# Performance work log

Measured on AMD Instinct MI355X. Metric: run time of the kernel, lower is better.

The kernel has to match this reference:

```python
import jax, jax.numpy as jnp
import numpy as np
import math

KEY_DIM = 16
COMPAT_FACTOR = 1.0 / math.sqrt(KEY_DIM)


def setup_inputs() -> dict:
    key = jax.random.key(0)
    k1, k2, k3, k4, k5 = jax.random.split(key, 5)
    B, G, D, H, K, V = 4, 2048, 128, 8, 16, 16
    h = jax.random.normal(k1, (B, G, D), dtype=jnp.float32)
    # mask: 1 = masked-out (attention forced to zero), 0 = attend
    mask = jax.random.randint(k2, (G, G), 0, 2, dtype=jnp.int32)
    # xavier_uniform over (input_dim, key_dim) fan per head
    lim_qk = math.sqrt(6.0 / (D + K))
    lim_v = math.sqrt(6.0 / (D + V))
    W_Q = jax.random.uniform(k3, (H, D, K), jnp.float32, -lim_qk, lim_qk)
    W_K = jax.random.uniform(k4, (H, D, K), jnp.float32, -lim_qk, lim_qk)
    W_V = jax.random.uniform(k5, (H, D, V), jnp.float32, -lim_v, lim_v)
    return {"h": h, "mask": mask, "W_Q": W_Q, "W_K": W_K, "W_V": W_V}


def reference(h, mask, W_Q, W_K, W_V):
    # h: [B, G, D]; W_Q/W_K: [H, D, K]; W_V: [H, D, V]; mask: [G, G] (1 = masked)
    q = jnp.einsum("bgd,hdk->bhgk", h, W_Q)  # [B, H, G, K]
    k = jnp.einsum("bgd,hdk->bhgk", h, W_K)  # [B, H, G, K]
    v = jnp.einsum("bgd,hdv->bhgv", h, W_V)  # [B, H, G, V]
    compat = COMPAT_FACTOR * jnp.einsum("bhqk,bhgk->bhqg", q, k)  # [B, H, G, G]
    masked = (mask > 0)[None, None, :, :]  # broadcast over batch, heads
    neg = jnp.finfo(compat.dtype).min
    compat = jnp.where(masked, neg, compat)
    attn = jax.nn.softmax(compat, axis=-1)
    # post-softmax hard zeroing at masked positions (as in the original)
    attn = jnp.where(masked, jnp.zeros((), attn.dtype), attn)
    h_p = jnp.einsum("bhqg,bhgv->bhqv", attn, v)  # [B, H, G, V]
    return h_p
```

## Files before the change

kernel.cpp:

```cpp
#include <hip/hip_runtime.h>
#include <hip/hip_bf16.h>

#define GG 2048
#define DD 128
#define HH 8
#define BH 32

typedef _Float16 h2 __attribute__((ext_vector_type(2)));
typedef _Float16 h4 __attribute__((ext_vector_type(4)));
typedef _Float16 h8 __attribute__((ext_vector_type(8)));
typedef __attribute__((ext_vector_type(4))) float f32x4;
typedef unsigned short u16;
typedef unsigned int   u32;
typedef unsigned char  u8;
typedef unsigned long long u64;

#define QSCALE 0.36067376022224085f

#define OFF_Q 0u
#define OFF_K (2u << 20)
#define OFF_V (4u << 20)
#define OFF_M (6u << 20)
#define OFF_H 6815744u
#define OFF_W 8912896u

#if __has_builtin(__builtin_amdgcn_exp2f)
#define EXP2F(x) __builtin_amdgcn_exp2f(x)
#else
#define EXP2F(x) exp2f(x)
#endif

#define MFMA16(a, b, c) __builtin_amdgcn_mfma_f32_16x16x16f16(a, b, c, 0, 0, 0)

__global__ __launch_bounds__(256) void prep_kernel(
    const float* __restrict__ h, const int* __restrict__ mask,
    const float* __restrict__ WQ, const float* __restrict__ WK,
    const float* __restrict__ WV,
    _Float16* __restrict__ hF, _Float16* __restrict__ Wc, u8* __restrict__ mbt)
{
  const int blk = blockIdx.x, tid = threadIdx.x;
  if (blk < 512) {
    int i = (blk * 256 + tid) * 8;
    float4 a = *(const float4*)(h + i);
    float4 b = *(const float4*)(h + i + 4);
    h8 o = { (_Float16)a.x, (_Float16)a.y, (_Float16)a.z, (_Float16)a.w,
             (_Float16)b.x, (_Float16)b.y, (_Float16)b.z, (_Float16)b.w };
    *(h8*)(hF + i) = o;
  } else if (blk < 704) {
    int j = (blk - 512) * 256 + tid;
    int hh = j / (48 * DD);
    int r  = j % (48 * DD);
    int n  = r / DD;
    int d  = r % DD;
    float val;
    if (n < 16)      val = WQ[((size_t)hh * DD + d) * 16 + n] * QSCALE;
    else if (n < 32) val = WK[((size_t)hh * DD + d) * 16 + (n - 16)];
    else             val = WV[((size_t)hh * DD + d) * 16 + (n - 32)];
    Wc[j] = (_Float16)val;
  } else {
    int t = (blk - 704) * 256 + tid;
    const int* m = mask + (size_t)t * 8;
    int4 m0 = *(const int4*)m;
    int4 m1 = *(const int4*)(m + 4);
    u32 byte = (m0.x > 0) | ((m0.y > 0) << 1) | ((m0.z > 0) << 2) | ((m0.w > 0) << 3)
             | ((m1.x > 0) << 4) | ((m1.y > 0) << 5) | ((m1.z > 0) << 6) | ((m1.w > 0) << 7);
    int q  = t >> 8;
    int k8 = t & 255;
    mbt[(size_t)(k8 >> 4) * (GG * 16) + (size_t)q * 16 + (k8 & 15)] = (u8)byte;
  }
}

__global__ __launch_bounds__(64) void proj_mfma(
    const _Float16* __restrict__ hF, const _Float16* __restrict__ Wc,
    _Float16* __restrict__ Qh, _Float16* __restrict__ Kh, _Float16* __restrict__ Vt)
{
  const int bh = blockIdx.x >> 5;
  const int gt = blockIdx.x & 31;
  const int b  = bh >> 3;
  const int hh = bh & (HH - 1);
  const int lane = threadIdx.x;
  const int col  = lane & 15;
  const int quad = lane >> 4;
  const int g0 = gt * 64;

  const _Float16* hb = hF + (size_t)b * GG * DD;
  const _Float16* W  = Wc + (size_t)hh * 48 * DD;

  f32x4 acc[4][3];
  #pragma unroll
  for (int mt = 0; mt < 4; ++mt)
    #pragma unroll
    for (int nt = 0; nt < 3; ++nt)
      acc[mt][nt] = (f32x4){0.f, 0.f, 0.f, 0.f};

  #pragma unroll
  for (int s = 0; s < 4; ++s) {
    h8 a[4], bw[3];
    #pragma unroll
    for (int mt = 0; mt < 4; ++mt)
      a[mt] = *(const h8*)(hb + (size_t)(g0 + mt * 16 + col) * DD + s * 32 + quad * 8);
    #pragma unroll
    for (int nt = 0; nt < 3; ++nt)
      bw[nt] = *(const h8*)(W + (size_t)(nt * 16 + col) * DD + s * 32 + quad * 8);
    #pragma unroll
    for (int mt = 0; mt < 4; ++mt)
      #pragma unroll
      for (int nt = 0; nt < 3; ++nt)
        acc[mt][nt] = __builtin_amdgcn_mfma_f32_16x16x32_f16(a[mt], bw[nt], acc[mt][nt], 0, 0, 0);
  }

  #pragma unroll
  for (int mt = 0; mt < 4; ++mt) {
    #pragma unroll
    for (int r = 0; r < 4; ++r) {
      int g = g0 + mt * 16 + quad * 4 + r;
      Qh[((size_t)bh * GG + g) * 16 + col] = (_Float16)acc[mt][0][r];
      Kh[((size_t)bh * GG + g) * 16 + col] = (_Float16)acc[mt][1][r];
      Vt[((size_t)bh * 16 + col) * GG + g] = (_Float16)acc[mt][2][r];
    }
  }
}

__global__ __launch_bounds__(256) void attn_kernel(
    const _Float16* __restrict__ Qh, const _Float16* __restrict__ Kh,
    const _Float16* __restrict__ Vt, const u8* __restrict__ mbt,
    float* __restrict__ out)
{
  const int tid = threadIdx.x, wave = tid >> 6, lane = tid & 63;
  const int col = lane & 15, quad = lane >> 4;
  const int bh = blockIdx.x & 31;
  const int qb = (blockIdx.x >> 5) * 128 + wave * 32;

  const h4 qf0 = *(const h4*)(Qh + ((size_t)bh * GG + qb + col) * 16 + quad * 4);
  const h4 qf1 = *(const h4*)(Qh + ((size_t)bh * GG + qb + 16 + col) * 16 + quad * 4);

  const _Float16* Kb = Kh + (size_t)bh * GG * 16;
  const _Float16* Vb = Vt + ((size_t)bh * 16 + col) * GG;
  const u8* mr0 = mbt + (size_t)(qb + col) * 16;
  const u8* mr1 = mbt + (size_t)(qb + 16 + col) * 16;

  f32x4 acc0 = {0.f,0.f,0.f,0.f}, acc1 = {0.f,0.f,0.f,0.f};
  const f32x4 cinit = {-4.f, -4.f, -4.f, -4.f};
  float ls0 = 0.f, ls1 = 0.f;
  const int shq = quad * 4;

  for (int g8 = 0; g8 < 16; ++g8) {
    const size_t goff = (size_t)g8 * (GG * 16);
    uint4 mv0 = *(const uint4*)(mr0 + goff);
    uint4 mv1 = *(const uint4*)(mr1 + goff);
    u64 wa0 = (u64)mv0.x | ((u64)mv0.y << 32);
    u64 wa1 = (u64)mv0.z | ((u64)mv0.w << 32);
    u64 wb0 = (u64)mv1.x | ((u64)mv1.y << 32);
    u64 wb1 = (u64)mv1.z | ((u64)mv1.w << 32);

    h4 kf[8], vf[8];
    #pragma unroll
    for (int t = 0; t < 8; ++t) {
      const int kb = g8 * 128 + t * 16;
      kf[t] = *(const h4*)(Kb + (size_t)(kb + col) * 16 + shq);
      vf[t] = *(const h4*)(Vb + kb + shq);
    }

    #pragma unroll
    for (int t = 0; t < 8; ++t) {
      f32x4 s0 = MFMA16(kf[t], qf0, cinit);
      f32x4 s1 = MFMA16(kf[t], qf1, cinit);
      const int sh = (t & 3) * 16 + shq;
      u32 b0 = (u32)(((t < 4) ? wa0 : wa1) >> sh) & 0xFu;
      u32 b1 = (u32)(((t < 4) ? wb0 : wb1) >> sh) & 0xFu;

      float a0 = (b0 & 1u) ? 0.f : EXP2F(s0[0]);
      float a1 = (b0 & 2u) ? 0.f : EXP2F(s0[1]);
      float a2 = (b0 & 4u) ? 0.f : EXP2F(s0[2]);
      float a3 = (b0 & 8u) ? 0.f : EXP2F(s0[3]);
      float c0 = (b1 & 1u) ? 0.f : EXP2F(s1[0]);
      float c1 = (b1 & 2u) ? 0.f : EXP2F(s1[1]);
      float c2 = (b1 & 4u) ? 0.f : EXP2F(s1[2]);
      float c3 = (b1 & 8u) ? 0.f : EXP2F(s1[3]);
      ls0 += (a0 + a1) + (a2 + a3);
      ls1 += (c0 + c1) + (c2 + c3);

      h2 pa01 = __builtin_bit_cast(h2, __builtin_amdgcn_cvt_pkrtz(a0, a1));
      h2 pa23 = __builtin_bit_cast(h2, __builtin_amdgcn_cvt_pkrtz(a2, a3));
      h4 pf0 = __builtin_shufflevector(pa01, pa23, 0, 1, 2, 3);
      h2 pc01 = __builtin_bit_cast(h2, __builtin_amdgcn_cvt_pkrtz(c0, c1));
      h2 pc23 = __builtin_bit_cast(h2, __builtin_amdgcn_cvt_pkrtz(c2, c3));
      h4 pf1 = __builtin_shufflevector(pc01, pc23, 0, 1, 2, 3);

      acc0 = MFMA16(vf[t], pf0, acc0);
      acc1 = MFMA16(vf[t], pf1, acc1);
    }
  }

  float l0 = ls0; l0 += __shfl_xor(l0, 16, 64); l0 += __shfl_xor(l0, 32, 64);
  float l1 = ls1; l1 += __shfl_xor(l1, 16, 64); l1 += __shfl_xor(l1, 32, 64);
  float r0 = (l0 > 0.f) ? (1.f / l0) : 0.f;
  float r1 = (l1 > 0.f) ? (1.f / l1) : 0.f;

  float4 o0 = { acc0[0] * r0, acc0[1] * r0, acc0[2] * r0, acc0[3] * r0 };
  float4 o1 = { acc1[0] * r1, acc1[1] * r1, acc1[2] * r1, acc1[3] * r1 };
  *(float4*)(out + ((size_t)bh * GG + qb + col) * 16 + quad * 4) = o0;
  *(float4*)(out + ((size_t)bh * GG + qb + 16 + col) * 16 + quad * 4) = o1;
}

extern "C" void kernel_launch(void* const* d_in, const int* in_sizes, int n_in,
                              void* d_out, int out_size, void* d_ws, size_t ws_size,
                              hipStream_t stream) {
  const float* h    = (const float*)d_in[0];
  const int*   mask = (const int*)d_in[1];
  const float* WQ   = (const float*)d_in[2];
  const float* WK   = (const float*)d_in[3];
  const float* WV   = (const float*)d_in[4];
  float* out = (float*)d_out;
  char* ws = (char*)d_ws;
  _Float16* Qh = (_Float16*)(ws + OFF_Q);
  _Float16* Kh = (_Float16*)(ws + OFF_K);
  _Float16* Vt = (_Float16*)(ws + OFF_V);
  u8*       mbt = (u8*)(ws + OFF_M);
  _Float16* hF = (_Float16*)(ws + OFF_H);
  _Float16* Wc = (_Float16*)(ws + OFF_W);

  hipLaunchKernelGGL(prep_kernel, dim3(2752), dim3(256), 0, stream,
                     h, mask, WQ, WK, WV, hF, Wc, mbt);
  hipLaunchKernelGGL(proj_mfma, dim3(BH * (GG / 64)), dim3(64), 0, stream,
                     hF, Wc, Qh, Kh, Vt);
  hipLaunchKernelGGL(attn_kernel, dim3(BH * (GG / 128)), dim3(256), 0, stream,
                     Qh, Kh, Vt, mbt, out);
}
```

Baseline: 123.6 us.

## Split attention key range across two wave groups and sum row totals via MFMA

The attention block grows to 512 threads: each group of four waves processes half of the key range for the same query rows, and the partial outputs and row sums are combined through shared memory after a barrier. The row-sum accumulation moves from scalar adds plus cross-lane shuffles to an extra MFMA against a ones vector. This doubles the number of waves available to hide latency on a grid of only 512 blocks. In exchange it doubles the MFMA count in the inner loop and adds an LDS reduction and a barrier.

Result: slower. 126.4 us (+2.3%).

```diff
diff --git a/kernel.cpp b/kernel.cpp
--- a/kernel.cpp
+++ b/kernel.cpp
@@ -121,15 +121,19 @@
   }
 }
 
-__global__ __launch_bounds__(256) void attn_kernel(
+__global__ __launch_bounds__(512, 4) void attn_kernel(
     const _Float16* __restrict__ Qh, const _Float16* __restrict__ Kh,
     const _Float16* __restrict__ Vt, const u8* __restrict__ mbt,
     float* __restrict__ out)
 {
-  const int tid = threadIdx.x, wave = tid >> 6, lane = tid & 63;
+  __shared__ float Lacc[4][32][17];
+  __shared__ float Ll[4][32];
+  const int tid = threadIdx.x, wv = tid >> 6, lane = tid & 63;
+  const int g   = wv & 3;
+  const int kh  = wv >> 2;
   const int col = lane & 15, quad = lane >> 4;
   const int bh = blockIdx.x & 31;
-  const int qb = (blockIdx.x >> 5) * 128 + wave * 32;
+  const int qb = (blockIdx.x >> 5) * 128 + g * 32;
 
   const h4 qf0 = *(const h4*)(Qh + ((size_t)bh * GG + qb + col) * 16 + quad * 4);
   const h4 qf1 = *(const h4*)(Qh + ((size_t)bh * GG + qb + 16 + col) * 16 + quad * 4);
@@ -140,12 +144,14 @@
   const u8* mr1 = mbt + (size_t)(qb + 16 + col) * 16;
 
   f32x4 acc0 = {0.f,0.f,0.f,0.f}, acc1 = {0.f,0.f,0.f,0.f};
+  f32x4 lacc0 = {0.f,0.f,0.f,0.f}, lacc1 = {0.f,0.f,0.f,0.f};
   const f32x4 cinit = {-4.f, -4.f, -4.f, -4.f};
-  float ls0 = 0.f, ls1 = 0.f;
+  const h4 ones = {(_Float16)1.f, (_Float16)1.f, (_Float16)1.f, (_Float16)1.f};
   const int shq = quad * 4;
 
-  for (int g8 = 0; g8 < 16; ++g8) {
-    const size_t goff = (size_t)g8 * (GG * 16);
+  for (int g8 = 0; g8 < 8; ++g8) {
+    const int gg = kh * 8 + g8;
+    const size_t goff = (size_t)gg * (GG * 16);
     uint4 mv0 = *(const uint4*)(mr0 + goff);
     uint4 mv1 = *(const uint4*)(mr1 + goff);
     u64 wa0 = (u64)mv0.x | ((u64)mv0.y << 32);
@@ -156,7 +162,7 @@
     h4 kf[8], vf[8];
     #pragma unroll
     for (int t = 0; t < 8; ++t) {
-      const int kb = g8 * 128 + t * 16;
+      const int kb = gg * 128 + t * 16;
       kf[t] = *(const h4*)(Kb + (size_t)(kb + col) * 16 + shq);
       vf[t] = *(const h4*)(Vb + kb + shq);
     }
@@ -177,8 +183,6 @@
       float c1 = (b1 & 2u) ? 0.f : EXP2F(s1[1]);
       float c2 = (b1 & 4u) ? 0.f : EXP2F(s1[2]);
       float c3 = (b1 & 8u) ? 0.f : EXP2F(s1[3]);
-      ls0 += (a0 + a1) + (a2 + a3);
-      ls1 += (c0 + c1) + (c2 + c3);
 
       h2 pa01 = __builtin_bit_cast(h2, __builtin_amdgcn_cvt_pkrtz(a0, a1));
       h2 pa23 = __builtin_bit_cast(h2, __builtin_amdgcn_cvt_pkrtz(a2, a3));
@@ -189,18 +193,40 @@
 
       acc0 = MFMA16(vf[t], pf0, acc0);
       acc1 = MFMA16(vf[t], pf1, acc1);
-    }
-  }
-
-  float l0 = ls0; l0 += __shfl_xor(l0, 16, 64); l0 += __shfl_xor(l0, 32, 64);
-  float l1 = ls1; l1 += __shfl_xor(l1, 16, 64); l1 += __shfl_xor(l1, 32, 64);
-  float r0 = (l0 > 0.f) ? (1.f / l0) : 0.f;
-  float r1 = (l1 > 0.f) ? (1.f / l1) : 0.f;
-
-  float4 o0 = { acc0[0] * r0, acc0[1] * r0, acc0[2] * r0, acc0[3] * r0 };
-  float4 o1 = { acc1[0] * r1, acc1[1] * r1, acc1[2] * r1, acc1[3] * r1 };
-  *(float4*)(out + ((size_t)bh * GG + qb + col) * 16 + quad * 4) = o0;
-  *(float4*)(out + ((size_t)bh * GG + qb + 16 + col) * 16 + quad * 4) = o1;
+      lacc0 = MFMA16(ones, pf0, lacc0);
+      lacc1 = MFMA16(ones, pf1, lacc1);
+    }
+  }
+
+  const float l0 = lacc0[0];
+  const float l1 = lacc1[0];
+
+  if (kh == 0) {
+    #pragma unroll
+    for (int r = 0; r < 4; ++r) {
+      Lacc[g][col][shq + r]      = acc0[r];
+      Lacc[g][col + 16][shq + r] = acc1[r];
+    }
+    if (quad == 0) { Ll[g][col] = l0; Ll[g][col + 16] = l1; }
+  }
+  __syncthreads();
+  if (kh == 1) {
+    float la = Ll[g][col] + l0;
+    float lb = Ll[g][col + 16] + l1;
+    float ra = (la > 0.f) ? (1.f / la) : 0.f;
+    float rb = (lb > 0.f) ? (1.f / lb) : 0.f;
+    float4 o0, o1;
+    o0.x = (Lacc[g][col][shq + 0] + acc0[0]) * ra;
+    o0.y = (Lacc[g][col][shq + 1] + acc0[1]) * ra;
+    o0.z = (Lacc[g][col][shq + 2] + acc0[2]) * ra;
+    o0.w = (Lacc[g][col][shq + 3] + acc0[3]) * ra;
+    o1.x = (Lacc[g][col + 16][shq + 0] + acc1[0]) * rb;
+    o1.y = (Lacc[g][col + 16][shq + 1] + acc1[1]) * rb;
+    o1.z = (Lacc[g][col + 16][shq + 2] + acc1[2]) * rb;
+    o1.w = (Lacc[g][col + 16][shq + 3] + acc1[3]) * rb;
+    *(float4*)(out + ((size_t)bh * GG + qb + col) * 16 + shq) = o0;
+    *(float4*)(out + ((size_t)bh * GG + qb + 16 + col) * 16 + shq) = o1;
+  }
 }
 
 extern "C" void kernel_launch(void* const* d_in, const int* in_sizes, int n_in,
@@ -224,6 +250,6 @@
                      h, mask, WQ, WK, WV, hF, Wc, mbt);
   hipLaunchKernelGGL(proj_mfma, dim3(BH * (GG / 64)), dim3(64), 0, stream,
                      hF, Wc, Qh, Kh, Vt);
-  hipLaunchKernelGGL(attn_kernel, dim3(BH * (GG / 128)), dim3(256), 0, stream,
+  hipLaunchKernelGGL(attn_kernel, dim3(BH * (GG / 128)), dim3(512), 0, stream,
                      Qh, Kh, Vt, mbt, out);
 }
```
